# Optimization experiments

Hardware: AMD Instinct MI355X
Metric: run time of the kernel (lower is better)

Reference implementation:

```python
import jax, jax.numpy as jnp
import numpy as np

N_QUBITS = 10
T_STEPS = 10
NDATA = 1024
DIM = 2 ** N_QUBITS
PI = float(np.pi)


def setup_inputs() -> dict:
    key = jax.random.key(0)
    k1, k2, k3, k4, k5 = jax.random.split(key, 5)
    # random complex amplitudes (normalized to unit states inside reference)
    inputs_re = jax.random.normal(k1, (NDATA, DIM), dtype=jnp.float32)
    inputs_im = jax.random.normal(k2, (NDATA, DIM), dtype=jnp.float32)
    # diffusion noise schedule diff_hs (t,) in (0,1]
    diff_hs = jax.random.uniform(k5, (T_STEPS,), dtype=jnp.float32, minval=0.1, maxval=1.0)
    # var_1 = diff_hs.repeat(3n) in torch == tile -> index k scaled by diff_hs[k % t]
    var_1 = jnp.tile(diff_hs, 3 * N_QUBITS)                                  # (3*n*t,)
    phis = (jax.random.uniform(k3, (NDATA, 3 * N_QUBITS * T_STEPS), dtype=jnp.float32)
            * (PI / 4.0) - (PI / 8.0)) * var_1[None, :]
    gs = (jax.random.uniform(k4, (NDATA, T_STEPS), dtype=jnp.float32) * 0.2 + 0.4) * diff_hs[None, :]
    return {"inputs_re": inputs_re, "inputs_im": inputs_im, "phis": phis, "gs": gs}


def _apply_1q(psi, M, i):
    """Apply per-sample 2x2 gate M (B,2,2) on qubit i (qubit 0 = MSB) to psi (B, 2**n)."""
    left = 2 ** i
    right = 2 ** (N_QUBITS - 1 - i)
    s = psi.reshape(NDATA, left, 2, right)
    s = jnp.einsum('bxy,bayc->baxc', M, s)
    return s.reshape(NDATA, DIM)


def _scramble(inputs_re, inputs_im, phis, gs):
    n, t = N_QUBITS, T_STEPS
    psi = (inputs_re + 1j * inputs_im).astype(jnp.complex64)
    psi = psi / jnp.linalg.norm(psi, axis=1, keepdims=True)  # unit input states

    # precompute sum_{i<j} z_i z_j per basis state for the diagonal RZZ product
    idx = jnp.arange(DIM)
    bits = (idx[:, None] >> jnp.arange(n - 1, -1, -1)[None, :]) & 1  # (DIM, n), qubit0=MSB
    z = 1.0 - 2.0 * bits.astype(jnp.float32)
    zsum = z.sum(axis=1)
    pairsum = 0.5 * (zsum ** 2 - n)                                   # (DIM,)
    inv = 1.0 / (2.0 * np.sqrt(float(n)))

    for tt in range(t):
        base = 3 * n * tt
        for i in range(n):
            a = phis[:, base + i]            # first RZ angle
            th = phis[:, base + n + i]       # RY angle
            b = phis[:, base + 2 * n + i]    # second RZ angle
            c = jnp.cos(0.5 * th).astype(jnp.complex64)
            s = jnp.sin(0.5 * th).astype(jnp.complex64)
            ea_m = jnp.exp(-0.5j * a); ea_p = jnp.exp(0.5j * a)
            eb_m = jnp.exp(-0.5j * b); eb_p = jnp.exp(0.5j * b)
            # M = RZ(b) @ RY(th) @ RZ(a), per sample (B,2,2)
            M = jnp.stack([
                jnp.stack([eb_m * c * ea_m, -eb_m * s * ea_p], axis=-1),
                jnp.stack([eb_p * s * ea_m,  eb_p * c * ea_p], axis=-1),
            ], axis=-2)
            psi = _apply_1q(psi, M, i)
        # all RZZ(i,j, theta) gates are diagonal with shared theta -> single fused phase
        theta = (gs[:, tt] * inv).astype(jnp.complex64)
        psi = psi * jnp.exp(-0.5j * theta[:, None] * pairsum[None, :])
    return psi


def reference(inputs_re, inputs_im, phis, gs):
    psi = _scramble(inputs_re, inputs_im, phis, gs)
    return jnp.stack([psi.real, psi.imag])  # (2, Ndata, 2**n) float32
```

## Files before the change

kernel.cpp:

```cpp
#include <hip/hip_runtime.h>

#define NQ 10
#define TS 10
#define DIM 1024
#define ND 1024

typedef _Float16 h4 __attribute__((ext_vector_type(4)));
typedef __fp16  p2 __attribute__((ext_vector_type(2)));
typedef float f4 __attribute__((ext_vector_type(4)));

__device__ __forceinline__ f4 mfma16(h4 a, h4 b, f4 c) {
    return __builtin_amdgcn_mfma_f32_16x16x16f16(a, b, c, 0, 0, 0);
}
__device__ __forceinline__ h4 cvt_h4(f4 x) {
    p2 lo = __builtin_amdgcn_cvt_pkrtz(x[0], x[1]);
    p2 hi = __builtin_amdgcn_cvt_pkrtz(x[2], x[3]);
    h4 r; r[0] = lo[0]; r[1] = lo[1]; r[2] = hi[0]; r[3] = hi[1];
    return r;
}
__device__ __forceinline__ float hsel(int ob, int ib, float cq, float sq) {
    return (ob == ib) ? cq : (ob ? sq : -sq);
}

__global__ __launch_bounds__(64, 1) void qsim_kernel(
    const float* __restrict__ re_in, const float* __restrict__ im_in,
    const float* __restrict__ phis, const float* __restrict__ gs,
    float* __restrict__ out)
{
    const int sample = blockIdx.x;
    const int lane = threadIdx.x;
    const int quad = lane >> 4;
    const int cc = lane & 15;
    const int c3 = (cc >> 3) & 1, c2 = (cc >> 2) & 1, c1 = (cc >> 1) & 1, c0 = cc & 1;
    const int q1 = quad >> 1, q0 = quad & 1;

    const float* pr_in = re_in + sample * DIM;
    const float* pi_in = im_in + sample * DIM;
    const float* ph = phis + sample * (3 * NQ * TS);
    const float* gsp = gs + sample * TS;

    f4 Sr[4], Si[4];
    const int lbase = 256 * quad + cc;
#pragma unroll
    for (int n = 0; n < 4; ++n)
#pragma unroll
        for (int s = 0; s < 4; ++s) {
            Sr[n][s] = pr_in[lbase + 64 * s + 16 * n];
            Si[n][s] = pi_in[lbase + 64 * s + 16 * n];
        }

    const float inv = 0.15811388300841897f;
    float gk[TS];
#pragma unroll
    for (int t = 0; t < TS; ++t) gk[t] = -0.5f * (gsp[t] * inv);

    float nrm = 0.f;
#pragma unroll
    for (int n = 0; n < 4; ++n)
#pragma unroll
        for (int s = 0; s < 4; ++s) nrm += Sr[n][s] * Sr[n][s] + Si[n][s] * Si[n][s];
#pragma unroll
    for (int off = 32; off >= 1; off >>= 1) nrm += __shfl_xor(nrm, off, 64);
    const float scl = rsqrtf(nrm);
#pragma unroll
    for (int n = 0; n < 4; ++n) { Sr[n] *= scl; Si[n] *= scl; }

    float psv[4][4];
    const int pbase = __popc(quad) + __popc(cc);
#pragma unroll
    for (int n = 0; n < 4; ++n)
#pragma unroll
        for (int s = 0; s < 4; ++s) {
            const int p = pbase + __popc(n) + __popc(s);
            const int z = NQ - 2 * p;
            psv[n][s] = 0.5f * (float)(z * z - NQ);
        }
    const float fq1 = (float)q1, fq0 = (float)q0;
    const float fc3 = (float)c3, fc2 = (float)c2, fc1 = (float)c1, fc0 = (float)c0;

    float DCP[4][4], DSP[4][4];
    h4 gb; h4 hb[4][4];
    float bcur[NQ];

    auto make_trig = [&](const float* v, float kcur, float dcp[4][4], float dsp[4][4]) {
        float sv = 0.f;
#pragma unroll
        for (int i = 0; i < NQ; ++i) sv += v[i];
        float base = fmaf(-0.5f, sv, 0.f);
        base = fmaf(fq1, v[0], base); base = fmaf(fq0, v[1], base);
        base = fmaf(fc3, v[6], base); base = fmaf(fc2, v[7], base);
        base = fmaf(fc1, v[8], base); base = fmaf(fc0, v[9], base);
        const float addS[4] = {0.f, v[3], v[2], v[2] + v[3]};
        const float addN[4] = {0.f, v[5], v[4], v[4] + v[5]};
#pragma unroll
        for (int n = 0; n < 4; ++n)
#pragma unroll
            for (int s = 0; s < 4; ++s) {
                const float phi = fmaf(kcur, psv[n][s], base + addN[n] + addS[s]);
                float sp, cp;
                __sincosf(phi, &sp, &cp);
                dcp[n][s] = cp;
                dsp[n][s] = sp;
            }
    };
    auto make_tiles = [&](const float* th_src, h4& gbo, h4 hbo[4][4]) {
        float C[NQ], S[NQ];
#pragma unroll
        for (int g = 0; g < NQ; ++g) {
            float sg, cg;
            __sincosf(0.5f * th_src[g], &sg, &cg);
            S[g] = sg; C[g] = cg;
        }
        {
            const float f01 = hsel(c3, q1, C[0], S[0]) * hsel(c2, q0, C[1], S[1]);
            float e[4];
#pragma unroll
            for (int s = 0; s < 4; ++s)
                e[s] = f01 * hsel(c1, s >> 1, C[2], S[2]) * hsel(c0, s & 1, C[3], S[3]);
            p2 lo = __builtin_amdgcn_cvt_pkrtz(e[0], e[1]);
            p2 hi = __builtin_amdgcn_cvt_pkrtz(e[2], e[3]);
            gbo[0] = lo[0]; gbo[1] = lo[1]; gbo[2] = hi[0]; gbo[3] = hi[1];
        }
        const float F67 = hsel(c3, q1, C[6], S[6]) * hsel(c2, q0, C[7], S[7]);
        float F89[4];
#pragma unroll
        for (int s = 0; s < 4; ++s)
            F89[s] = F67 * hsel(c1, s >> 1, C[8], S[8]) * hsel(c0, s & 1, C[9], S[9]);
#pragma unroll
        for (int n = 0; n < 4; ++n)
#pragma unroll
            for (int j = 0; j < 4; ++j) {
                const float F45 = hsel(n >> 1, j >> 1, C[4], S[4])
                                * hsel(n & 1,  j & 1,  C[5], S[5]);
                p2 lo = __builtin_amdgcn_cvt_pkrtz(F45 * F89[0], F45 * F89[1]);
                p2 hi = __builtin_amdgcn_cvt_pkrtz(F45 * F89[2], F45 * F89[3]);
                hbo[n][j][0] = lo[0]; hbo[n][j][1] = lo[1];
                hbo[n][j][2] = hi[0]; hbo[n][j][3] = hi[1];
            }
    };

    {
        float phs0[30];
#pragma unroll
        for (int j = 0; j < 30; ++j) phs0[j] = ph[j];
        make_trig(&phs0[0], 0.f, DCP, DSP);
        make_tiles(&phs0[10], gb, hb);
#pragma unroll
        for (int i = 0; i < NQ; ++i) bcur[i] = phs0[20 + i];
    }
    float pipe[2][30];
#pragma unroll
    for (int j = 0; j < 30; ++j) pipe[0][j] = ph[30 + j];

    const f4 zf4 = {0.f, 0.f, 0.f, 0.f};

#pragma unroll
    for (int tt = 0; tt < TS; ++tt) {
#pragma unroll
        for (int n = 0; n < 4; ++n)
#pragma unroll
            for (int s = 0; s < 4; ++s) {
                const float cp = DCP[n][s], sp = DSP[n][s];
                const float xr = Sr[n][s], xi = Si[n][s];
                Sr[n][s] = cp * xr - sp * xi;
                Si[n][s] = sp * xr + cp * xi;
            }

        if (tt + 2 < TS) {
#pragma unroll
            for (int j = 0; j < 30; ++j) pipe[(tt + 1) & 1][j] = ph[30 * (tt + 2) + j];
        }

        h4 ar[4], ai[4];
#pragma unroll
        for (int n = 0; n < 4; ++n) { ar[n] = cvt_h4(Sr[n]); ai[n] = cvt_h4(Si[n]); }
        f4 Tr[4], Ti[4];
#pragma unroll
        for (int n = 0; n < 4; ++n) {
            Tr[n] = mfma16(ar[n], gb, zf4);
            Ti[n] = mfma16(ai[n], gb, zf4);
        }
        h4 tr[4], ti[4];
#pragma unroll
        for (int n = 0; n < 4; ++n) { tr[n] = cvt_h4(Tr[n]); ti[n] = cvt_h4(Ti[n]); }
#pragma unroll
        for (int n = 0; n < 4; ++n) {
            f4 accr = zf4, acci = zf4;
#pragma unroll
            for (int j = 0; j < 4; ++j) {
                accr = mfma16(tr[j], hb[n][j], accr);
                acci = mfma16(ti[j], hb[n][j], acci);
            }
            Sr[n] = accr;
            Si[n] = acci;
        }

        if (tt + 1 < TS) {
            const float* pN = pipe[tt & 1];
            float vN[NQ];
#pragma unroll
            for (int i = 0; i < NQ; ++i) vN[i] = pN[i] + bcur[i];
            make_trig(vN, gk[tt], DCP, DSP);
            make_tiles(&pN[10], gb, hb);
#pragma unroll
            for (int i = 0; i < NQ; ++i) bcur[i] = pN[20 + i];
        } else {
            make_trig(bcur, gk[TS - 1], DCP, DSP);
        }
    }

#pragma unroll
    for (int n = 0; n < 4; ++n)
#pragma unroll
        for (int s = 0; s < 4; ++s) {
            const float cp = DCP[n][s], sp = DSP[n][s];
            const float xr = Sr[n][s], xi = Si[n][s];
            Sr[n][s] = cp * xr - sp * xi;
            Si[n][s] = sp * xr + cp * xi;
        }

    float* outr = out + sample * DIM;
    float* outi = out + ND * DIM + sample * DIM;
#pragma unroll
    for (int n = 0; n < 4; ++n)
#pragma unroll
        for (int s = 0; s < 4; ++s) {
            outr[lbase + 64 * s + 16 * n] = Sr[n][s];
            outi[lbase + 64 * s + 16 * n] = Si[n][s];
        }
}

extern "C" void kernel_launch(void* const* d_in, const int* in_sizes, int n_in,
                              void* d_out, int out_size, void* d_ws, size_t ws_size,
                              hipStream_t stream) {
    const float* re_in = (const float*)d_in[0];
    const float* im_in = (const float*)d_in[1];
    const float* phis  = (const float*)d_in[2];
    const float* gs    = (const float*)d_in[3];
    float* out = (float*)d_out;
    qsim_kernel<<<ND, 64, 0, stream>>>(re_in, im_in, phis, gs, out);
}
```

Measured before the change: 77.90 us.

## Process two samples per wavefront to interleave independent MFMA chains

Each 64-thread block now handles two samples (blockIdx.x and blockIdx.x+512), and the grid is halved. The two samples' state updates, trig generation and MFMA chains are interleaved so independent work can hide MFMA and transcendental latency within one wave. The tt loop is no longer fully unrolled and phis loads go through an inline-asm v_mov, which forces them into VGPRs instead of scalar registers. The cost is roughly double the register pressure and only 512 waves, which may leave CUs underfilled on a 256-CU part.

```diff
diff --git a/kernel.cpp b/kernel.cpp
--- a/kernel.cpp
+++ b/kernel.cpp
@@ -21,49 +21,67 @@
 __device__ __forceinline__ float hsel(int ob, int ib, float cq, float sq) {
     return (ob == ib) ? cq : (ob ? sq : -sq);
 }
+__device__ __forceinline__ float vmov(float x) {
+    float y;
+    asm("v_mov_b32 %0, %1" : "=v"(y) : "v"(x));
+    return y;
+}
 
 __global__ __launch_bounds__(64, 1) void qsim_kernel(
     const float* __restrict__ re_in, const float* __restrict__ im_in,
     const float* __restrict__ phis, const float* __restrict__ gs,
     float* __restrict__ out)
 {
-    const int sample = blockIdx.x;
     const int lane = threadIdx.x;
     const int quad = lane >> 4;
     const int cc = lane & 15;
     const int c3 = (cc >> 3) & 1, c2 = (cc >> 2) & 1, c1 = (cc >> 1) & 1, c0 = cc & 1;
     const int q1 = quad >> 1, q0 = quad & 1;
 
-    const float* pr_in = re_in + sample * DIM;
-    const float* pi_in = im_in + sample * DIM;
-    const float* ph = phis + sample * (3 * NQ * TS);
-    const float* gsp = gs + sample * TS;
-
-    f4 Sr[4], Si[4];
+    const int smp[2] = {(int)blockIdx.x, (int)blockIdx.x + 512};
+    const float* prp[2]; const float* pip[2]; const float* php[2];
+#pragma unroll
+    for (int u = 0; u < 2; ++u) {
+        prp[u] = re_in + smp[u] * DIM;
+        pip[u] = im_in + smp[u] * DIM;
+        php[u] = phis + smp[u] * (3 * NQ * TS);
+    }
+
     const int lbase = 256 * quad + cc;
-#pragma unroll
-    for (int n = 0; n < 4; ++n)
-#pragma unroll
-        for (int s = 0; s < 4; ++s) {
-            Sr[n][s] = pr_in[lbase + 64 * s + 16 * n];
-            Si[n][s] = pi_in[lbase + 64 * s + 16 * n];
-        }
+
+    f4 Sr[2][4], Si[2][4];
+#pragma unroll
+    for (int u = 0; u < 2; ++u)
+#pragma unroll
+        for (int n = 0; n < 4; ++n)
+#pragma unroll
+            for (int s = 0; s < 4; ++s) {
+                Sr[u][n][s] = prp[u][lbase + 64 * s + 16 * n];
+                Si[u][n][s] = pip[u][lbase + 64 * s + 16 * n];
+            }
 
     const float inv = 0.15811388300841897f;
-    float gk[TS];
-#pragma unroll
-    for (int t = 0; t < TS; ++t) gk[t] = -0.5f * (gsp[t] * inv);
-
-    float nrm = 0.f;
-#pragma unroll
-    for (int n = 0; n < 4; ++n)
-#pragma unroll
-        for (int s = 0; s < 4; ++s) nrm += Sr[n][s] * Sr[n][s] + Si[n][s] * Si[n][s];
-#pragma unroll
-    for (int off = 32; off >= 1; off >>= 1) nrm += __shfl_xor(nrm, off, 64);
-    const float scl = rsqrtf(nrm);
-#pragma unroll
-    for (int n = 0; n < 4; ++n) { Sr[n] *= scl; Si[n] *= scl; }
+    float gkv[2][TS];
+#pragma unroll
+    for (int u = 0; u < 2; ++u)
+#pragma unroll
+        for (int t = 0; t < TS; ++t)
+            gkv[u][t] = -0.5f * (vmov(gs[smp[u] * TS + t]) * inv);
+
+#pragma unroll
+    for (int u = 0; u < 2; ++u) {
+        float nrm = 0.f;
+#pragma unroll
+        for (int n = 0; n < 4; ++n)
+#pragma unroll
+            for (int s = 0; s < 4; ++s)
+                nrm += Sr[u][n][s] * Sr[u][n][s] + Si[u][n][s] * Si[u][n][s];
+#pragma unroll
+        for (int off = 32; off >= 1; off >>= 1) nrm += __shfl_xor(nrm, off, 64);
+        const float scl = rsqrtf(nrm);
+#pragma unroll
+        for (int n = 0; n < 4; ++n) { Sr[u][n] *= scl; Si[u][n] *= scl; }
+    }
 
     float psv[4][4];
     const int pbase = __popc(quad) + __popc(cc);
@@ -78,11 +96,13 @@
     const float fq1 = (float)q1, fq0 = (float)q0;
     const float fc3 = (float)c3, fc2 = (float)c2, fc1 = (float)c1, fc0 = (float)c0;
 
-    float DCP[4][4], DSP[4][4];
-    h4 gb; h4 hb[4][4];
-    float bcur[NQ];
-
-    auto make_trig = [&](const float* v, float kcur, float dcp[4][4], float dsp[4][4]) {
+    float DCP[2][4][4], DSP[2][4][4];
+    h4 gb[2]; h4 hb[2][4][4];
+    float bcur[2][NQ];
+    float pipe[2][30];
+
+    auto make_trig = [&](const float* v, float kcur,
+                         float (&dcp)[4][4], float (&dsp)[4][4]) {
         float sv = 0.f;
 #pragma unroll
         for (int i = 0; i < NQ; ++i) sv += v[i];
@@ -103,7 +123,7 @@
                 dsp[n][s] = sp;
             }
     };
-    auto make_tiles = [&](const float* th_src, h4& gbo, h4 hbo[4][4]) {
+    auto make_tiles = [&](const float* th_src, h4& gbo, h4 (&hbo)[4][4]) {
         float C[NQ], S[NQ];
 #pragma unroll
         for (int g = 0; g < NQ; ++g) {
@@ -139,95 +159,110 @@
             }
     };
 
-    {
+#pragma unroll
+    for (int u = 0; u < 2; ++u) {
         float phs0[30];
 #pragma unroll
-        for (int j = 0; j < 30; ++j) phs0[j] = ph[j];
-        make_trig(&phs0[0], 0.f, DCP, DSP);
-        make_tiles(&phs0[10], gb, hb);
-#pragma unroll
-        for (int i = 0; i < NQ; ++i) bcur[i] = phs0[20 + i];
-    }
-    float pipe[2][30];
-#pragma unroll
-    for (int j = 0; j < 30; ++j) pipe[0][j] = ph[30 + j];
+        for (int j = 0; j < 30; ++j) phs0[j] = vmov(php[u][j]);
+        make_trig(&phs0[0], 0.f, DCP[u], DSP[u]);
+        make_tiles(&phs0[10], gb[u], hb[u]);
+#pragma unroll
+        for (int i = 0; i < NQ; ++i) bcur[u][i] = phs0[20 + i];
+    }
 
     const f4 zf4 = {0.f, 0.f, 0.f, 0.f};
 
-#pragma unroll
     for (int tt = 0; tt < TS; ++tt) {
+        if (tt + 1 < TS) {
+#pragma unroll
+            for (int u = 0; u < 2; ++u)
+#pragma unroll
+                for (int j = 0; j < 30; ++j)
+                    pipe[u][j] = vmov(php[u][30 * (tt + 1) + j]);
+        }
+
+#pragma unroll
+        for (int u = 0; u < 2; ++u)
+#pragma unroll
+            for (int n = 0; n < 4; ++n)
+#pragma unroll
+                for (int s = 0; s < 4; ++s) {
+                    const float cp = DCP[u][n][s], sp = DSP[u][n][s];
+                    const float xr = Sr[u][n][s], xi = Si[u][n][s];
+                    Sr[u][n][s] = cp * xr - sp * xi;
+                    Si[u][n][s] = sp * xr + cp * xi;
+                }
+
+        h4 ar[2][4], ai[2][4];
+#pragma unroll
+        for (int u = 0; u < 2; ++u)
+#pragma unroll
+            for (int n = 0; n < 4; ++n) {
+                ar[u][n] = cvt_h4(Sr[u][n]);
+                ai[u][n] = cvt_h4(Si[u][n]);
+            }
+        f4 Tr[2][4], Ti[2][4];
+#pragma unroll
+        for (int u = 0; u < 2; ++u)
+#pragma unroll
+            for (int n = 0; n < 4; ++n) {
+                Tr[u][n] = mfma16(ar[u][n], gb[u], zf4);
+                Ti[u][n] = mfma16(ai[u][n], gb[u], zf4);
+            }
+        h4 tr[2][4], ti[2][4];
+#pragma unroll
+        for (int u = 0; u < 2; ++u)
+#pragma unroll
+            for (int n = 0; n < 4; ++n) {
+                tr[u][n] = cvt_h4(Tr[u][n]);
+                ti[u][n] = cvt_h4(Ti[u][n]);
+            }
+#pragma unroll
+        for (int u = 0; u < 2; ++u)
+#pragma unroll
+            for (int n = 0; n < 4; ++n) {
+                f4 accr = zf4, acci = zf4;
+#pragma unroll
+                for (int j = 0; j < 4; ++j) {
+                    accr = mfma16(tr[u][j], hb[u][n][j], accr);
+                    acci = mfma16(ti[u][j], hb[u][n][j], acci);
+                }
+                Sr[u][n] = accr;
+                Si[u][n] = acci;
+            }
+
+        if (tt + 1 < TS) {
+#pragma unroll
+            for (int u = 0; u < 2; ++u) {
+                float vN[NQ];
+#pragma unroll
+                for (int i = 0; i < NQ; ++i) vN[i] = pipe[u][i] + bcur[u][i];
+                make_trig(vN, gkv[u][tt], DCP[u], DSP[u]);
+                make_tiles(&pipe[u][10], gb[u], hb[u]);
+#pragma unroll
+                for (int i = 0; i < NQ; ++i) bcur[u][i] = pipe[u][20 + i];
+            }
+        } else {
+#pragma unroll
+            for (int u = 0; u < 2; ++u)
+                make_trig(bcur[u], gkv[u][TS - 1], DCP[u], DSP[u]);
+        }
+    }
+
+#pragma unroll
+    for (int u = 0; u < 2; ++u) {
+        float* outr = out + smp[u] * DIM;
+        float* outi = out + ND * DIM + smp[u] * DIM;
 #pragma unroll
         for (int n = 0; n < 4; ++n)
 #pragma unroll
             for (int s = 0; s < 4; ++s) {
-                const float cp = DCP[n][s], sp = DSP[n][s];
-                const float xr = Sr[n][s], xi = Si[n][s];
-                Sr[n][s] = cp * xr - sp * xi;
-                Si[n][s] = sp * xr + cp * xi;
-            }
-
-        if (tt + 2 < TS) {
-#pragma unroll
-            for (int j = 0; j < 30; ++j) pipe[(tt + 1) & 1][j] = ph[30 * (tt + 2) + j];
-        }
-
-        h4 ar[4], ai[4];
-#pragma unroll
-        for (int n = 0; n < 4; ++n) { ar[n] = cvt_h4(Sr[n]); ai[n] = cvt_h4(Si[n]); }
-        f4 Tr[4], Ti[4];
-#pragma unroll
-        for (int n = 0; n < 4; ++n) {
-            Tr[n] = mfma16(ar[n], gb, zf4);
-            Ti[n] = mfma16(ai[n], gb, zf4);
-        }
-        h4 tr[4], ti[4];
-#pragma unroll
-        for (int n = 0; n < 4; ++n) { tr[n] = cvt_h4(Tr[n]); ti[n] = cvt_h4(Ti[n]); }
-#pragma unroll
-        for (int n = 0; n < 4; ++n) {
-            f4 accr = zf4, acci = zf4;
-#pragma unroll
-            for (int j = 0; j < 4; ++j) {
-                accr = mfma16(tr[j], hb[n][j], accr);
-                acci = mfma16(ti[j], hb[n][j], acci);
-            }
-            Sr[n] = accr;
-            Si[n] = acci;
-        }
-
-        if (tt + 1 < TS) {
-            const float* pN = pipe[tt & 1];
-            float vN[NQ];
-#pragma unroll
-            for (int i = 0; i < NQ; ++i) vN[i] = pN[i] + bcur[i];
-            make_trig(vN, gk[tt], DCP, DSP);
-            make_tiles(&pN[10], gb, hb);
-#pragma unroll
-            for (int i = 0; i < NQ; ++i) bcur[i] = pN[20 + i];
-        } else {
-            make_trig(bcur, gk[TS - 1], DCP, DSP);
-        }
-    }
-
-#pragma unroll
-    for (int n = 0; n < 4; ++n)
-#pragma unroll
-        for (int s = 0; s < 4; ++s) {
-            const float cp = DCP[n][s], sp = DSP[n][s];
-            const float xr = Sr[n][s], xi = Si[n][s];
-            Sr[n][s] = cp * xr - sp * xi;
-            Si[n][s] = sp * xr + cp * xi;
-        }
-
-    float* outr = out + sample * DIM;
-    float* outi = out + ND * DIM + sample * DIM;
-#pragma unroll
-    for (int n = 0; n < 4; ++n)
-#pragma unroll
-        for (int s = 0; s < 4; ++s) {
-            outr[lbase + 64 * s + 16 * n] = Sr[n][s];
-            outi[lbase + 64 * s + 16 * n] = Si[n][s];
-        }
+                const float cp = DCP[u][n][s], sp = DSP[u][n][s];
+                const float xr = Sr[u][n][s], xi = Si[u][n][s];
+                outr[lbase + 64 * s + 16 * n] = cp * xr - sp * xi;
+                outi[lbase + 64 * s + 16 * n] = sp * xr + cp * xi;
+            }
+    }
 }
 
 extern "C" void kernel_launch(void* const* d_in, const int* in_sizes, int n_in,
@@ -238,5 +273,5 @@
     const float* phis  = (const float*)d_in[2];
     const float* gs    = (const float*)d_in[3];
     float* out = (float*)d_out;
-    qsim_kernel<<<ND, 64, 0, stream>>>(re_in, im_in, phis, gs, out);
-}
+    qsim_kernel<<<ND / 2, 64, 0, stream>>>(re_in, im_in, phis, gs, out);
+}
```

Result: slower. 90.81 us (+16.6%).
